# Performance work log

Measured on AMD Instinct MI355X. Metric: run time of the kernel, lower is better.

Reference implementation:

```python
import jax, jax.numpy as jnp
import numpy as np

B, T, C, H = 4, 1024, 2048, 16
HD = C // H          # head dim = 128 (even, as RoPE requires)
BLOCK = 1024         # config.block_size == config.max_block_size
NEG = -1e30          # finite stand-in for -inf in the additive attention bias


def setup_inputs() -> dict:
    key = jax.random.key(0)
    k1, k2, k3, k4, k5 = jax.random.split(key, 5)
    x = jax.random.normal(k1, (B, T, C), jnp.float32)
    cumulative_scores = jax.random.uniform(k2, (B, T), jnp.float32)  # kept small: fed to exp()
    token_index = jax.random.randint(k3, (B, T), 0, BLOCK, dtype=jnp.int32)
    padding_mask = jnp.ones((B, T), jnp.int32)
    # xavier-ish scale so softmax doesn't saturate
    W_attn = jax.random.normal(k4, (C, 3 * C), jnp.float32) / np.sqrt(C)
    W_proj = jax.random.normal(k5, (C, C), jnp.float32) / np.sqrt(C)
    return dict(x=x, cumulative_scores=cumulative_scores, token_index=token_index,
                padding_mask=padding_mask, W_attn=W_attn, W_proj=W_proj)


def _rotate_half(a):
    a1, a2 = a[..., : HD // 2], a[..., HD // 2:]
    return jnp.concatenate([-a2, a1], axis=-1)


def reference(x, cumulative_scores, token_index, padding_mask, W_attn, W_proj):
    # QKV projection (bias=False per config)
    qkv = x @ W_attn                                  # (B,T,3C)
    q, k, v = jnp.split(qkv, 3, axis=2)
    heads = lambda a: a.reshape(B, T, H, HD).transpose(0, 2, 1, 3)  # (B,H,T,HD)
    q, k, v = heads(q), heads(k), heads(v)

    # input-dependent partial rotation positions (exact replica of the original
    # scatter: token_index (B,T) fancy-indexes the last axis of a (B,BLOCK)
    # buffer, so counts are summed over ALL batch rows, as in the source)
    counts = jnp.zeros((B, BLOCK), jnp.float32).at[..., token_index].add(1.0)
    t = jnp.cumsum(jnp.take_along_axis(1.0 / (counts + 1e-10), token_index, axis=-1), axis=-1)  # (B,T)

    # RoPE with per-token positions t (seq_dim=-2, offset 0 for both q and k)
    inv_freq = 1.0 / (10000.0 ** (jnp.arange(0, HD, 2, dtype=jnp.float32) / HD))
    freqs = jnp.einsum('bt,j->btj', t, inv_freq)
    emb = jnp.concatenate([freqs, freqs], axis=-1)[:, None, :, :]   # (B,1,T,HD)
    sin, cos = jnp.sin(emb), jnp.cos(emb)
    q = q * cos + _rotate_half(q) * sin
    k = k * cos + _rotate_half(k) * sin

    # 'fork' plan overrides on the last rotary channel
    q = q.at[..., -1].set(1.0)
    k = k.at[..., -1].set(jnp.broadcast_to(cumulative_scores[:, None, :], (B, H, T)))

    # V rescaled by exp(cumulative_scores)
    v = v * jnp.exp(cumulative_scores)[:, None, :, None]

    # causal + key-padding additive bias, SDPA with scale 1/sqrt(HD)
    keep = jnp.tril(jnp.ones((T, T), bool))[None, None] & padding_mask.astype(bool)[:, None, None, :]
    scores = jnp.einsum('bhqd,bhkd->bhqk', q, k) / np.sqrt(HD)
    scores = jnp.where(keep, scores, NEG)
    attn = jax.nn.softmax(scores, axis=-1)
    y = jnp.einsum('bhqk,bhkd->bhqd', attn, v)

    y = y.transpose(0, 2, 1, 3).reshape(B, T, C)
    return y @ W_proj
```

## Files before the change

### kernel.cpp

```cpp
#include <hip/hip_runtime.h>

#define BB 4
#define TT 1024
#define CCH 2048
#define HH 16
#define HDIM 128
#define NBLK 1024
#define MM (BB*TT)
#define N1 (3*CCH)
#define NQT 16

typedef _Float16 f16;
typedef _Float16 half8 __attribute__((ext_vector_type(8)));
typedef _Float16 half4 __attribute__((ext_vector_type(4)));
typedef float floatx4 __attribute__((ext_vector_type(4)));

__device__ __forceinline__ void g2lds16(const void* g, void* l) {
    __builtin_amdgcn_global_load_lds((const __attribute__((address_space(1))) void*)g,
                                     (__attribute__((address_space(3))) void*)l, 16, 0, 0);
}

__global__ void k_prep(const float* __restrict__ Wa, const float* __restrict__ Wp,
                       const float* __restrict__ x,
                       f16* __restrict__ WaT, f16* __restrict__ WpT,
                       f16* __restrict__ x16) {
    int z = blockIdx.z;
    if (z == 2) {
        int i = (blockIdx.y * 192 + blockIdx.x) * 256 + threadIdx.x + threadIdx.y * 32;
        if (i >= MM * CCH / 4) return;
        float4 v = ((const float4*)x)[i];
        union { ushort4 u; f16 h[4]; } o;
        o.h[0] = (f16)v.x; o.h[1] = (f16)v.y; o.h[2] = (f16)v.z; o.h[3] = (f16)v.w;
        ((ushort4*)x16)[i] = o.u;
        return;
    }
    const float* in = (z == 0) ? Wa : Wp;
    f16* out = (z == 0) ? WaT : WpT;
    int Cc = (z == 0) ? N1 : CCH;
    if (blockIdx.x * 32 >= Cc) return;
    __shared__ float tile[32][33];
    int c0 = blockIdx.x * 32, r0 = blockIdx.y * 32;
    int tx = threadIdx.x, ty = threadIdx.y;
#pragma unroll
    for (int k = 0; k < 4; k++) {
        int r = ty + k * 8;
        tile[r][tx] = in[(size_t)(r0 + r) * Cc + c0 + tx];
    }
    __syncthreads();
#pragma unroll
    for (int k = 0; k < 4; k++) {
        int r = ty + k * 8;
        out[(size_t)(c0 + r) * CCH + r0 + tx] = (f16)tile[tx][r];
    }
}

__global__ void k_trv(const f16* __restrict__ in, f16* __restrict__ out) {
    __shared__ f16 tile[32][34];
    int bh = blockIdx.z;
    int h0 = blockIdx.x * 32, t0 = blockIdx.y * 32;
    int tx = threadIdx.x, ty = threadIdx.y;
#pragma unroll
    for (int k = 0; k < 4; k++) {
        int t = ty + k * 8;
        tile[t][tx] = in[((size_t)bh * TT + t0 + t) * HDIM + h0 + tx];
    }
    __syncthreads();
#pragma unroll
    for (int k = 0; k < 4; k++) {
        int r = ty + k * 8;
        out[((size_t)bh * HDIM + h0 + r) * TT + t0 + tx] = tile[tx][r];
    }
}

__global__ void k_hist(const int* __restrict__ tok, int* __restrict__ cnt) {
    int i = blockIdx.x * blockDim.x + threadIdx.x;
    if (i < MM) atomicAdd(cnt + tok[i], 1);
}

__global__ __launch_bounds__(1024) void k_scan(const int* __restrict__ tok,
                                               const int* __restrict__ cnt,
                                               const int* __restrict__ pm,
                                               float* __restrict__ tpos,
                                               float* __restrict__ pb) {
    __shared__ float s[TT];
    int b = blockIdx.x, t = threadIdx.x;
    s[t] = 1.0f / ((float)cnt[tok[b * TT + t]] + 1e-10f);
    __syncthreads();
    for (int off = 1; off < TT; off <<= 1) {
        float add = (t >= off) ? s[t - off] : 0.0f;
        __syncthreads();
        s[t] += add;
        __syncthreads();
    }
    tpos[b * TT + t] = s[t];
    pb[b * TT + t] = pm[b * TT + t] ? 0.0f : -1e30f;
}

__global__ void k_rope(const float* __restrict__ tpos, float2* __restrict__ tab) {
    int i = blockIdx.x * 256 + threadIdx.x;
    int row = i >> 6, j = i & 63;
    float f = tpos[row] * expf((float)j * -0.14391156929f);
    float sn, cn; sincosf(f, &sn, &cn);
    tab[i] = make_float2(cn, sn);
}

#define BAR() __builtin_amdgcn_s_barrier()
#define RDA(S, base, ck) do { _Pragma("unroll") for (int m_ = 0; m_ < 4; m_++) \
    S[m_] = *(const half8*)((base) + aoffb + (m_ << 11) + (ck)); } while (0)
#define RDB(S, base, ck) do { _Pragma("unroll") for (int n_ = 0; n_ < 4; n_++) \
    S[n_] = *(const half8*)((base) + bofs[n_] + (ck)); } while (0)
#define STAGEA(t, base) do { _Pragma("unroll") for (int k_ = 0; k_ < 4; k_++) \
    g2lds16(Ab + (size_t)(k_ * 64) * 2048 + ((t) << 6) + srcr, \
            (base) + (w * 8 + k_ * 64) * 128); } while (0)
#define STAGEB(t, base) do { _Pragma("unroll") for (int k_ = 0; k_ < 2; k_++) \
    g2lds16(Bb + (size_t)(k_ * 64) * 2048 + ((t) << 6) + srcr, \
            (base) + (w * 8 + k_ * 64) * 128); } while (0)
#define MF16(SA, SB) do { _Pragma("unroll") for (int m_ = 0; m_ < 4; m_++) \
    _Pragma("unroll") for (int n_ = 0; n_ < 4; n_++) \
    acc[m_][n_] = __builtin_amdgcn_mfma_f32_16x16x32_f16(SA[m_], SB[n_], acc[m_][n_], 0, 0, 0); } while (0)

template <int MODE>
__global__ __launch_bounds__(512, 2) void k_gemm8(const f16* __restrict__ A,
                                                  const f16* __restrict__ Bt,
                                                  float* __restrict__ Cp,
                                                  const float2* __restrict__ tab,
                                                  const float* __restrict__ cs,
                                                  f16* __restrict__ qr,
                                                  f16* __restrict__ kr,
                                                  f16* __restrict__ vsc) {
    const float SCALE = 0.08838834764831845f;
    const int NBN = MODE ? 48 : 16;
    const int NWG = MODE ? 768 : 256;
    const int CPX = NWG >> 3;
    __shared__ __align__(16) f16 As[3 * 16384];
    __shared__ __align__(16) f16 Bs[3 * 8192];

    int bid = blockIdx.x;
    int s = (bid & 7) * CPX + (bid >> 3);
    int bm = s / NBN, bn = s % NBN;

    int tid = threadIdx.x;
    int w = tid >> 6, lane = tid & 63, quad = lane >> 4, l16 = lane & 15;
    int wm = w & 3, wn = w >> 2;

    const f16* Ab = A + (size_t)(bm << 8) * 2048;
    const f16* Bb = Bt + (size_t)(bn << 7) * 2048;

    int rl = lane >> 3, cl = lane & 7;
    int gl = (cl - rl) & 7;
    int srcr = (w * 8 + rl) * 2048 + gl * 8;

    const int aoffb = (wm * 64 + l16) << 7;
    const int bofs[4] = { (wn * 32 + l16) << 7,        (wn * 32 + 64 + l16) << 7,
                          (wn * 32 + 16 + l16) << 7,   (wn * 32 + 80 + l16) << 7 };
    const int ck0 = ((quad + l16) & 7) << 4;
    const int ck1 = ck0 ^ 64;

    floatx4 acc[4][4];
#pragma unroll
    for (int i = 0; i < 4; i++)
#pragma unroll
        for (int j = 0; j < 4; j++) acc[i][j] = (floatx4){0.f, 0.f, 0.f, 0.f};

    half8 S0a[4], S1a[4];
    half8 S0b[4], S1b[4];

    char* a0 = (char*)As; char* a1 = a0 + 32768; char* a2 = a0 + 65536;
    char* b0 = (char*)Bs; char* b1 = b0 + 16384; char* b2 = b0 + 32768;

    STAGEA(0, a0); STAGEB(0, b0);
    STAGEA(1, a1); STAGEB(1, b1);
    asm volatile("s_waitcnt vmcnt(6)" ::: "memory");
    BAR();
    RDA(S0a, a0, ck0); RDB(S0b, b0, ck0);

#pragma unroll 1
    for (int t = 0; t < 32; ++t) {
        RDA(S1a, a0, ck1); RDB(S1b, b0, ck1);
        if (t + 2 < 32) { STAGEA(t + 2, a2); STAGEB(t + 2, b2); }
        __builtin_amdgcn_s_setprio(1); MF16(S0a, S0b); __builtin_amdgcn_s_setprio(0);
        if (t < 30) { asm volatile("s_waitcnt vmcnt(6)" ::: "memory"); }
        else        { asm volatile("s_waitcnt vmcnt(0)" ::: "memory"); }
        BAR();
        if (t < 31) { RDA(S0a, a1, ck0); RDB(S0b, b1, ck0); }
        __builtin_amdgcn_s_setprio(1); MF16(S1a, S1b); __builtin_amdgcn_s_setprio(0);
        BAR();
        char* ta = a0; a0 = a1; a1 = a2; a2 = ta;
        char* tb = b0; b0 = b1; b1 = b2; b2 = tb;
    }

    if (MODE == 0) {
#pragma unroll
        for (int mf = 0; mf < 4; mf++)
#pragma unroll
            for (int nf = 0; nf < 4; nf++) {
                int col = (bn << 7) + ((nf & 1) << 6) + wn * 32 + ((nf >> 1) << 4) + l16;
#pragma unroll
                for (int r = 0; r < 4; r++) {
                    int row = (bm << 8) + wm * 64 + mf * 16 + (quad << 2) + r;
                    Cp[(size_t)row * CCH + col] = acc[mf][nf][r];
                }
            }
    } else {
        int type = bn >> 4;
        int h = bn & 15;
        if (type < 2) {
            f16* outp = (type == 0) ? qr : kr;
#pragma unroll
            for (int mf = 0; mf < 4; mf++)
#pragma unroll
                for (int r = 0; r < 4; r++) {
                    int row = (bm << 8) + wm * 64 + mf * 16 + (quad << 2) + r;
#pragma unroll
                    for (int p = 0; p < 2; p++) {
                        int d1 = wn * 32 + p * 16 + l16;
                        float2 tc = tab[row * 64 + d1];
                        float a1v = acc[mf][2 * p][r], a2v = acc[mf][2 * p + 1][r];
                        float o1 = a1v * tc.x - a2v * tc.y;
                        float o2 = a2v * tc.x + a1v * tc.y;
                        if (type == 0) {
                            if (d1 == 63) o2 = 1.0f;
                            o1 *= SCALE; o2 *= SCALE;
                        } else {
                            if (d1 == 63) o2 = cs[row];
                        }
                        size_t ob = ((size_t)((row >> 10) * HH + h) * TT + (row & 1023)) * HDIM + d1;
                        outp[ob] = (f16)o1;
                        outp[ob + 64] = (f16)o2;
                    }
                }
        } else {
#pragma unroll
            for (int mf = 0; mf < 4; mf++)
#pragma unroll
                for (int r = 0; r < 4; r++) {
                    int row = (bm << 8) + wm * 64 + mf * 16 + (quad << 2) + r;
                    float ve = __expf(cs[row]);
#pragma unroll
                    for (int nf = 0; nf < 4; nf++) {
                        int d = ((nf & 1) << 6) + wn * 32 + ((nf >> 1) << 4) + l16;
                        size_t ob = ((size_t)((row >> 10) * HH + h) * TT + (row & 1023)) * HDIM + d;
                        vsc[ob] = (f16)(acc[mf][nf][r] * ve);
                    }
                }
        }
    }
}

__global__ __launch_bounds__(256) void k_attn(const f16* __restrict__ qr,
                                              const f16* __restrict__ kr,
                                              const f16* __restrict__ vt,
                                              const float* __restrict__ pb,
                                              f16* __restrict__ y) {
    __shared__ __align__(16) f16 Ks[64 * 136];
    __shared__ __align__(16) f16 Vs[128 * 72];
    __shared__ float pbs[64];
    int p = blockIdx.x & (NQT / 2 - 1);
    int bh = blockIdx.x >> 3;
    int b = bh >> 4, h = bh & 15;
    int tid = threadIdx.x;
    int w = tid >> 6, lane = tid & 63, quad = lane >> 4, l16 = lane & 15;
#pragma unroll
    for (int pass = 0; pass < 2; pass++) {
        int qt = pass ? (NQT - 1 - p) : p;
        int q0 = qt << 6;
        int qg = q0 + w * 16 + l16;
        const f16* Qp = qr + ((size_t)bh * TT + qg) * HDIM;
        half8 qf[4];
#pragma unroll
        for (int kc = 0; kc < 4; kc++) qf[kc] = *(const half8*)&Qp[kc * 32 + (quad << 3)];
        floatx4 O[8];
#pragma unroll
        for (int i = 0; i < 8; i++) O[i] = (floatx4){0.f, 0.f, 0.f, 0.f};
        float mx = -1e30f, ls = 0.f;
        for (int kt = 0; kt <= qt; kt++) {
            __syncthreads();
            const f16* Kb = kr + ((size_t)bh * TT + (kt << 6)) * HDIM;
            const f16* Vb = vt + (size_t)bh * HDIM * TT + (kt << 6);
#pragma unroll
            for (int i = 0; i < 4; i++) {
                int seg = tid + (i << 8);
                int krow = seg >> 4, kcol = (seg & 15) << 3;
                *(uint4*)&Ks[krow * 136 + kcol] = *(const uint4*)&Kb[(size_t)krow * HDIM + kcol];
                int vrow = seg >> 3, vcol = (seg & 7) << 3;
                *(uint4*)&Vs[vrow * 72 + vcol] = *(const uint4*)&Vb[(size_t)vrow * TT + vcol];
            }
            if (tid < 64) pbs[tid] = pb[b * TT + (kt << 6) + tid];
            __syncthreads();
            floatx4 Sv[4];
#pragma unroll
            for (int mc = 0; mc < 4; mc++) Sv[mc] = (floatx4){0.f, 0.f, 0.f, 0.f};
#pragma unroll
            for (int kc = 0; kc < 4; kc++)
#pragma unroll
                for (int mc = 0; mc < 4; mc++) {
                    half8 kf = *(const half8*)&Ks[(mc * 16 + l16) * 136 + kc * 32 + (quad << 3)];
                    Sv[mc] = __builtin_amdgcn_mfma_f32_16x16x32_f16(kf, qf[kc], Sv[mc], 0, 0, 0);
                }
            float pv[4][4];
            float mnew = mx;
#pragma unroll
            for (int mc = 0; mc < 4; mc++) {
                float4 pbv = *(const float4*)&pbs[mc * 16 + (quad << 2)];
#pragma unroll
                for (int i = 0; i < 4; i++) {
                    int kv = (kt << 6) + mc * 16 + (quad << 2) + i;
                    float s = (kv <= qg) ? Sv[mc][i] + ((const float*)&pbv)[i] : -1e30f;
                    pv[mc][i] = s;
                    mnew = fmaxf(mnew, s);
                }
            }
            mnew = fmaxf(mnew, __shfl_xor(mnew, 16));
            mnew = fmaxf(mnew, __shfl_xor(mnew, 32));
            float al = __expf(mx - mnew);
            mx = mnew;
            float psum = 0.f;
#pragma unroll
            for (int mc = 0; mc < 4; mc++)
#pragma unroll
                for (int i = 0; i < 4; i++) {
                    float e = __expf(pv[mc][i] - mnew);
                    pv[mc][i] = e;
                    psum += e;
                }
            psum += __shfl_xor(psum, 16);
            psum += __shfl_xor(psum, 32);
            ls = ls * al + psum;
#pragma unroll
            for (int hm = 0; hm < 8; hm++)
#pragma unroll
                for (int i = 0; i < 4; i++) O[hm][i] *= al;
            half4 pf[4];
#pragma unroll
            for (int mc = 0; mc < 4; mc++) {
                pf[mc][0] = (f16)pv[mc][0]; pf[mc][1] = (f16)pv[mc][1];
                pf[mc][2] = (f16)pv[mc][2]; pf[mc][3] = (f16)pv[mc][3];
            }
#pragma unroll
            for (int mc = 0; mc < 4; mc++)
#pragma unroll
                for (int hm = 0; hm < 8; hm++) {
                    half4 vf = *(const half4*)&Vs[(hm * 16 + l16) * 72 + mc * 16 + (quad << 2)];
                    O[hm] = __builtin_amdgcn_mfma_f32_16x16x16f16(vf, pf[mc], O[hm], 0, 0, 0);
                }
        }
        float inv = 1.0f / ls;
#pragma unroll
        for (int hm = 0; hm < 8; hm++) {
            half4 ov;
#pragma unroll
            for (int i = 0; i < 4; i++) ov[i] = (f16)(O[hm][i] * inv);
            *(half4*)&y[((size_t)b * TT + qg) * CCH + h * HDIM + hm * 16 + (quad << 2)] = ov;
        }
        __syncthreads();
    }
}

extern "C" void kernel_launch(void* const* d_in, const int* in_sizes, int n_in,
                              void* d_out, int out_size, void* d_ws, size_t ws_size,
                              hipStream_t stream) {
    const float* x   = (const float*)d_in[0];
    const float* cs  = (const float*)d_in[1];
    const int*   tok = (const int*)d_in[2];
    const int*   pm  = (const int*)d_in[3];
    const float* Wa  = (const float*)d_in[4];
    const float* Wp  = (const float*)d_in[5];
    float* out = (float*)d_out;
    char* ws = (char*)d_ws;

    f16* x16 = (f16*)(ws + 0);
    f16* WaT = (f16*)(ws + 16777216);
    f16* vt  = (f16*)(ws + 41943040);
    f16* WpT = (f16*)(ws + 58720256);
    float2* tab = (float2*)(ws + 67108864);
    f16* qr  = (f16*)(ws + 92274688);
    f16* kr  = (f16*)(ws + 109051904);
    f16* vsc = (f16*)(ws + 125829120);
    int*   cnt  = (int*)(ws + 142606336);
    float* tpos = (float*)(ws + 142610432);
    float* pb   = (float*)(ws + 142626816);
    f16* y   = x16;

    hipMemsetAsync(cnt, 0, NBLK * sizeof(int), stream);
    k_hist<<<MM / 256, 256, 0, stream>>>(tok, cnt);
    k_scan<<<BB, TT, 0, stream>>>(tok, cnt, pm, tpos, pb);
    k_rope<<<MM * 64 / 256, 256, 0, stream>>>(tpos, tab);
    k_prep<<<dim3(N1 / 32, CCH / 32, 3), dim3(32, 8), 0, stream>>>(Wa, Wp, x, WaT, WpT, x16);
    k_gemm8<1><<<768, 512, 0, stream>>>(x16, WaT, nullptr, tab, cs, qr, kr, vsc);
    k_trv<<<dim3(4, 32, BB * HH), dim3(32, 8), 0, stream>>>(vsc, vt);
    k_attn<<<BB * HH * (NQT / 2), 256, 0, stream>>>(qr, kr, vt, pb, y);
    k_gemm8<0><<<256, 512, 0, stream>>>(y, WpT, out, nullptr, nullptr, nullptr, nullptr, nullptr);
}
```

Before: 388.2 us.

## Double-buffer K/V tiles in attention with register prefetch of next tile

The attention kernel now keeps two LDS buffers for the K, V and bias tiles. At the start of each iteration it loads the next tile from global memory into registers, computes on the current buffer, then writes the prefetched data into the other buffer, so there is one barrier per iteration instead of two. The causal mask check is also limited to the diagonal tile. The cost is twice the LDS and more registers held live across the MFMA work, which may lower occupancy.

```diff
diff --git a/kernel.cpp b/kernel.cpp
--- a/kernel.cpp
+++ b/kernel.cpp
@@ -252,14 +252,16 @@
                                               const f16* __restrict__ vt,
                                               const float* __restrict__ pb,
                                               f16* __restrict__ y) {
-    __shared__ __align__(16) f16 Ks[64 * 136];
-    __shared__ __align__(16) f16 Vs[128 * 72];
-    __shared__ float pbs[64];
+    __shared__ __align__(16) f16 Ks[2][64 * 136];
+    __shared__ __align__(16) f16 Vs[2][128 * 72];
+    __shared__ float pbs[2][64];
     int p = blockIdx.x & (NQT / 2 - 1);
     int bh = blockIdx.x >> 3;
     int b = bh >> 4, h = bh & 15;
     int tid = threadIdx.x;
     int w = tid >> 6, lane = tid & 63, quad = lane >> 4, l16 = lane & 15;
+    const int krow0 = tid >> 4, kcol0 = (tid & 15) << 3;
+    const int vrow0 = tid >> 3, vcol0 = (tid & 7) << 3;
 #pragma unroll
     for (int pass = 0; pass < 2; pass++) {
         int qt = pass ? (NQT - 1 - p) : p;
@@ -273,20 +275,36 @@
 #pragma unroll
         for (int i = 0; i < 8; i++) O[i] = (floatx4){0.f, 0.f, 0.f, 0.f};
         float mx = -1e30f, ls = 0.f;
+        {
+            const f16* Kb = kr + (size_t)bh * TT * HDIM;
+            const f16* Vb = vt + (size_t)bh * HDIM * TT;
+#pragma unroll
+            for (int i = 0; i < 4; i++) {
+                *(uint4*)&Ks[0][(krow0 + i * 16) * 136 + kcol0] =
+                    *(const uint4*)&Kb[(size_t)(krow0 + i * 16) * HDIM + kcol0];
+                *(uint4*)&Vs[0][(vrow0 + i * 32) * 72 + vcol0] =
+                    *(const uint4*)&Vb[(size_t)(vrow0 + i * 32) * TT + vcol0];
+            }
+            if (tid < 64) pbs[0][tid] = pb[b * TT + tid];
+        }
+        __syncthreads();
+        int cur = 0;
         for (int kt = 0; kt <= qt; kt++) {
-            __syncthreads();
-            const f16* Kb = kr + ((size_t)bh * TT + (kt << 6)) * HDIM;
-            const f16* Vb = vt + (size_t)bh * HDIM * TT + (kt << 6);
-#pragma unroll
-            for (int i = 0; i < 4; i++) {
-                int seg = tid + (i << 8);
-                int krow = seg >> 4, kcol = (seg & 15) << 3;
-                *(uint4*)&Ks[krow * 136 + kcol] = *(const uint4*)&Kb[(size_t)krow * HDIM + kcol];
-                int vrow = seg >> 3, vcol = (seg & 7) << 3;
-                *(uint4*)&Vs[vrow * 72 + vcol] = *(const uint4*)&Vb[(size_t)vrow * TT + vcol];
-            }
-            if (tid < 64) pbs[tid] = pb[b * TT + (kt << 6) + tid];
-            __syncthreads();
+            uint4 kreg[4], vreg[4];
+            float pbnext = 0.f;
+            const bool have = (kt < qt);
+            if (have) {
+                const f16* Kb = kr + ((size_t)bh * TT + ((kt + 1) << 6)) * HDIM;
+                const f16* Vb = vt + (size_t)bh * HDIM * TT + ((kt + 1) << 6);
+#pragma unroll
+                for (int i = 0; i < 4; i++) {
+                    kreg[i] = *(const uint4*)&Kb[(size_t)(krow0 + i * 16) * HDIM + kcol0];
+                    vreg[i] = *(const uint4*)&Vb[(size_t)(vrow0 + i * 32) * TT + vcol0];
+                }
+                if (tid < 64) pbnext = pb[b * TT + ((kt + 1) << 6) + tid];
+            }
+            const f16* Kl = Ks[cur];
+            const f16* Vl = Vs[cur];
             floatx4 Sv[4];
 #pragma unroll
             for (int mc = 0; mc < 4; mc++) Sv[mc] = (floatx4){0.f, 0.f, 0.f, 0.f};
@@ -294,20 +312,33 @@
             for (int kc = 0; kc < 4; kc++)
 #pragma unroll
                 for (int mc = 0; mc < 4; mc++) {
-                    half8 kf = *(const half8*)&Ks[(mc * 16 + l16) * 136 + kc * 32 + (quad << 3)];
+                    half8 kf = *(const half8*)&Kl[(mc * 16 + l16) * 136 + kc * 32 + (quad << 3)];
                     Sv[mc] = __builtin_amdgcn_mfma_f32_16x16x32_f16(kf, qf[kc], Sv[mc], 0, 0, 0);
                 }
             float pv[4][4];
             float mnew = mx;
-#pragma unroll
-            for (int mc = 0; mc < 4; mc++) {
-                float4 pbv = *(const float4*)&pbs[mc * 16 + (quad << 2)];
-#pragma unroll
-                for (int i = 0; i < 4; i++) {
-                    int kv = (kt << 6) + mc * 16 + (quad << 2) + i;
-                    float s = (kv <= qg) ? Sv[mc][i] + ((const float*)&pbv)[i] : -1e30f;
-                    pv[mc][i] = s;
-                    mnew = fmaxf(mnew, s);
+            if (kt == qt) {
+#pragma unroll
+                for (int mc = 0; mc < 4; mc++) {
+                    float4 pbv = *(const float4*)&pbs[cur][mc * 16 + (quad << 2)];
+#pragma unroll
+                    for (int i = 0; i < 4; i++) {
+                        int kv = (kt << 6) + mc * 16 + (quad << 2) + i;
+                        float s = (kv <= qg) ? Sv[mc][i] + ((const float*)&pbv)[i] : -1e30f;
+                        pv[mc][i] = s;
+                        mnew = fmaxf(mnew, s);
+                    }
+                }
+            } else {
+#pragma unroll
+                for (int mc = 0; mc < 4; mc++) {
+                    float4 pbv = *(const float4*)&pbs[cur][mc * 16 + (quad << 2)];
+#pragma unroll
+                    for (int i = 0; i < 4; i++) {
+                        float s = Sv[mc][i] + ((const float*)&pbv)[i];
+                        pv[mc][i] = s;
+                        mnew = fmaxf(mnew, s);
+                    }
                 }
             }
             mnew = fmaxf(mnew, __shfl_xor(mnew, 16));
@@ -340,9 +371,20 @@
             for (int mc = 0; mc < 4; mc++)
 #pragma unroll
                 for (int hm = 0; hm < 8; hm++) {
-                    half4 vf = *(const half4*)&Vs[(hm * 16 + l16) * 72 + mc * 16 + (quad << 2)];
+                    half4 vf = *(const half4*)&Vl[(hm * 16 + l16) * 72 + mc * 16 + (quad << 2)];
                     O[hm] = __builtin_amdgcn_mfma_f32_16x16x16f16(vf, pf[mc], O[hm], 0, 0, 0);
                 }
+            if (have) {
+                int nxt = cur ^ 1;
+#pragma unroll
+                for (int i = 0; i < 4; i++) {
+                    *(uint4*)&Ks[nxt][(krow0 + i * 16) * 136 + kcol0] = kreg[i];
+                    *(uint4*)&Vs[nxt][(vrow0 + i * 32) * 72 + vcol0] = vreg[i];
+                }
+                if (tid < 64) pbs[nxt][tid] = pbnext;
+            }
+            __syncthreads();
+            cur ^= 1;
         }
         float inv = 1.0f / ls;
 #pragma unroll
```

Result: faster. 371.1 us (-4.4%).
